# Kernel optimization log

Measured on AMD Instinct MI355X. Metric: run time of the kernel, lower is better.

## Reference

```python
import jax, jax.numpy as jnp
import numpy as np

V, E, H = 32000, 256, 256  # vocab, embed dim, encoder hidden (decoder hidden = 2H)
B, S, T = 64, 32, 32


def gru_cell(x, h, W_ih, W_hh, b_ih, b_hh):
    # PyTorch GRU cell math. x: (B, in), h: (B, Hd)
    gi = x @ W_ih.T + b_ih
    gh = h @ W_hh.T + b_hh
    i_r, i_z, i_n = jnp.split(gi, 3, axis=-1)
    h_r, h_z, h_n = jnp.split(gh, 3, axis=-1)
    r = jax.nn.sigmoid(i_r + h_r)
    z = jax.nn.sigmoid(i_z + h_z)
    n = jnp.tanh(i_n + r * h_n)
    return (1.0 - z) * n + z * h


def setup_inputs() -> dict:
    key = jax.random.key(0)
    ks = jax.random.split(key, 20)
    s = 0.05
    emb_enc = jax.random.normal(ks[0], (V, E), jnp.float32) * s
    emb_enc = emb_enc.at[0].set(0.0)  # padding_idx=0
    emb_dec = jax.random.normal(ks[1], (V, E), jnp.float32) * s
    emb_dec = emb_dec.at[0].set(0.0)
    inp = {
        "src": jax.random.randint(ks[2], (B, S), 0, V),
        "trg": jax.random.randint(ks[3], (B, T), 0, V),
        "emb_enc": emb_enc,
        # encoder bidirectional GRU (single layer)
        "W_ih_f": jax.random.normal(ks[4], (3 * H, E), jnp.float32) * s,
        "W_hh_f": jax.random.normal(ks[5], (3 * H, H), jnp.float32) * s,
        "b_ih_f": jnp.zeros((3 * H,), jnp.float32),
        "b_hh_f": jnp.zeros((3 * H,), jnp.float32),
        "W_ih_b": jax.random.normal(ks[6], (3 * H, E), jnp.float32) * s,
        "W_hh_b": jax.random.normal(ks[7], (3 * H, H), jnp.float32) * s,
        "b_ih_b": jnp.zeros((3 * H,), jnp.float32),
        "b_hh_b": jnp.zeros((3 * H,), jnp.float32),
        "emb_dec": emb_dec,
        # decoder GRU: input E + 2H, hidden 2H
        "W_ih_d": jax.random.normal(ks[8], (3 * 2 * H, E + 2 * H), jnp.float32) * s,
        "W_hh_d": jax.random.normal(ks[9], (3 * 2 * H, 2 * H), jnp.float32) * s,
        "b_ih_d": jnp.zeros((3 * 2 * H,), jnp.float32),
        "b_hh_d": jnp.zeros((3 * 2 * H,), jnp.float32),
        "fc_W": jax.random.normal(ks[10], (V, 2 * H), jnp.float32) * s,
        "fc_b": jnp.zeros((V,), jnp.float32),
    }
    return inp


def _forward(src, trg, emb_enc, W_ih_f, W_hh_f, b_ih_f, b_hh_f,
             W_ih_b, W_hh_b, b_ih_b, b_hh_b, emb_dec,
             W_ih_d, W_hh_d, b_ih_d, b_hh_d, fc_W, fc_b):
    b, s = src.shape
    t = trg.shape[1]
    x = emb_enc[src]                      # (B,S,E)
    xs = jnp.swapaxes(x, 0, 1)            # (S,B,E)
    h0 = jnp.zeros((b, H), x.dtype)

    def fstep(h, xt):
        h = gru_cell(xt, h, W_ih_f, W_hh_f, b_ih_f, b_hh_f)
        return h, None

    def bstep(h, xt):
        h = gru_cell(xt, h, W_ih_b, W_hh_b, b_ih_b, b_hh_b)
        return h, None

    hf, _ = jax.lax.scan(fstep, h0, xs)
    hb, _ = jax.lax.scan(bstep, h0, xs[::-1])
    context = jnp.concatenate([hf, hb], axis=-1)   # (B,2H) = final bidir hidden

    # teacher_forcing_ratio = 1.0 -> decoder input at step t is trg[:, t-1]
    dec_in = jnp.swapaxes(trg[:, :-1], 0, 1)       # (T-1, B)

    def dstep(h, tok):
        xt = jnp.concatenate([emb_dec[tok], context], axis=-1)  # (B, E+2H)
        h = gru_cell(xt, h, W_ih_d, W_hh_d, b_ih_d, b_hh_d)
        logits = h @ fc_W.T + fc_b                              # (B, V)
        return h, logits

    _, logits = jax.lax.scan(dstep, context, dec_in)  # (T-1, B, V)
    logits = jnp.swapaxes(logits, 0, 1)                # (B, T-1, V)
    outputs = jnp.concatenate(
        [jnp.zeros((b, 1, fc_W.shape[0]), logits.dtype), logits], axis=1)
    return outputs


def reference(src, trg, emb_enc, W_ih_f, W_hh_f, b_ih_f, b_hh_f,
              W_ih_b, W_hh_b, b_ih_b, b_hh_b, emb_dec,
              W_ih_d, W_hh_d, b_ih_d, b_hh_d, fc_W, fc_b):
    return _forward(src, trg, emb_enc, W_ih_f, W_hh_f, b_ih_f, b_hh_f,
                    W_ih_b, W_hh_b, b_ih_b, b_hh_b, emb_dec,
                    W_ih_d, W_hh_d, b_ih_d, b_hh_d, fc_W, fc_b)
```

## Files before the change

kernel.cpp:

```cpp
#include <hip/hip_runtime.h>
#include <cmath>

typedef _Float16 f16;
typedef _Float16 f16x4 __attribute__((ext_vector_type(4)));
typedef _Float16 f16x8 __attribute__((ext_vector_type(8)));
typedef float f32x4 __attribute__((ext_vector_type(4)));
typedef unsigned u32x4 __attribute__((ext_vector_type(4)));
typedef unsigned long long u64;

static constexpr u64 SENT = 0xFFFFFFFFFFFFFFFFULL;

union V4 { u32x4 u; f16x8 h; };

typedef __attribute__((address_space(3))) void lds_t;
typedef const __attribute__((address_space(1))) void gbl_t;

static constexpr size_t OFF_WIHF = 0;
static constexpr size_t OFF_WHHF = OFF_WIHF + 768UL*256*2;
static constexpr size_t OFF_WIHB = OFF_WHHF + 768UL*256*2;
static constexpr size_t OFF_WHHB = OFF_WIHB + 768UL*256*2;
static constexpr size_t OFF_WIHD = OFF_WHHB + 768UL*256*2;
static constexpr size_t OFF_WHHD = OFF_WIHD + 1536UL*768*2;
static constexpr size_t OFF_FCW  = OFF_WHHD + 1536UL*512*2;
static constexpr size_t OFF_XENC = OFF_FCW  + 32000UL*512*2;
static constexpr size_t OFF_XDEC = OFF_XENC + 2048UL*256*2;
static constexpr size_t OFF_GIF  = OFF_XDEC + 1984UL*256*2;
static constexpr size_t OFF_GIB  = OFF_GIF  + 2048UL*768*4;
static constexpr size_t OFF_GITOK= OFF_GIB  + 2048UL*768*4;
static constexpr size_t OFF_CTX32= OFF_GITOK+ 1984UL*1536*4;
static constexpr size_t OFF_CTX16= OFF_CTX32+ 64UL*512*4;
static constexpr size_t OFF_HPP  = OFF_CTX16+ 64UL*512*2;
static constexpr size_t OFF_HALL = OFF_HPP  + 2UL*32*64*256*2;

__device__ __forceinline__ float sigmoidf_(float x) {
  return __builtin_amdgcn_rcpf(1.f + __expf(-x));
}
__device__ __forceinline__ float tanhf_(float x) {
  float xc = fminf(fmaxf(x, -10.f), 10.f);
  float e = __expf(2.f * xc);
  return (e - 1.f) * __builtin_amdgcn_rcpf(e + 1.f);
}

__device__ __forceinline__ void wait_vm0() {
  asm volatile("s_waitcnt vmcnt(0)" ::: "memory");
  __builtin_amdgcn_sched_barrier(0);
}
__device__ __forceinline__ void sth4(f16* p, float a, float b, float c, float d) {
  union { u64 u; f16 h[4]; } t;
  t.h[0] = (f16)a; t.h[1] = (f16)b; t.h[2] = (f16)c; t.h[3] = (f16)d;
  __hip_atomic_store((u64*)p, t.u, __ATOMIC_RELAXED, __HIP_MEMORY_SCOPE_AGENT);
}

__global__ void k_init(const int* __restrict__ srct, const int* __restrict__ trgt,
                       const float* __restrict__ embe, const float* __restrict__ embd,
                       const float* __restrict__ wihf, const float* __restrict__ whhf,
                       const float* __restrict__ wihb, const float* __restrict__ whhb,
                       const float* __restrict__ wihd, const float* __restrict__ whhd,
                       const float* __restrict__ fcw,
                       f16* dWihf, f16* dWhhf, f16* dWihb, f16* dWhhb,
                       f16* dWihd, f16* dWhhd, f16* dFcw,
                       f16* __restrict__ Xenc, f16* __restrict__ Xdec,
                       f16* __restrict__ hpp, f16* __restrict__ Hall,
                       float* __restrict__ out) {
  int b = blockIdx.x, tid = threadIdx.x;
  if (b < 1024) {
    long t = (long)b * 256 + tid;
    const long stride = 1024L * 256;
    for (long i = t; i < 4032L * 64; i += stride) {
      int row = (int)(i >> 6), j4 = (int)(i & 63);
      const float* e; f16* d; int tok;
      if (row < 2048) {
        int s = row >> 6, bb = row & 63;
        tok = srct[bb * 32 + s]; e = embe; d = Xenc + (long)row * 256;
      } else {
        int rd = row - 2048; int tt = rd >> 6, bb = rd & 63;
        tok = trgt[bb * 32 + tt]; e = embd; d = Xdec + (long)rd * 256;
      }
      float4 v = ((const float4*)(e + (long)tok * 256))[j4];
      f16x4 o; o.x = (f16)v.x; o.y = (f16)v.y; o.z = (f16)v.z; o.w = (f16)v.w;
      ((f16x4*)d)[j4] = o;
    }
    for (long i = t; i < 64L * 8000; i += stride) {
      long bb = i / 8000, j = i % 8000;
      ((float4*)(out + bb * 1024000L))[j] = make_float4(0.f, 0.f, 0.f, 0.f);
    }
    u64* H8 = (u64*)Hall;
    if (t < 253952) H8[t] = SENT;
    u64* P8 = (u64*)hpp;
    if (t < 4096) { P8[t] = 0ULL; P8[131072 + t] = 0ULL; }
    if (t < 126976) { P8[4096 + t] = SENT; P8[131072 + 4096 + t] = SENT; }
  } else {
    long cb = b - 1024;
    const long stride = 4672L * 256;
    for (long i = cb * 256 + tid; i < 4784128L; i += stride) {
      const float* s; f16* d; long j = i;
      if (j < 49152L)        { s = wihf; d = dWihf; }
      else if (j < 98304L)   { s = whhf; d = dWhhf; j -= 49152L; }
      else if (j < 147456L)  { s = wihb; d = dWihb; j -= 98304L; }
      else if (j < 196608L)  { s = whhb; d = dWhhb; j -= 147456L; }
      else if (j < 491520L)  { s = wihd; d = dWihd; j -= 196608L; }
      else if (j < 688128L)  { s = whhd; d = dWhhd; j -= 491520L; }
      else                   { s = fcw;  d = dFcw;  j -= 688128L; }
      float4 v = ((const float4*)s)[j];
      f16x4 o; o.x = (f16)v.x; o.y = (f16)v.y; o.z = (f16)v.z; o.w = (f16)v.w;
      ((f16x4*)d)[j] = o;
    }
  }
}

__device__ __forceinline__ void gemm_body(int bx, int by,
                                          const f16* __restrict__ A, int lda,
                                          const f16* __restrict__ B, int ldb,
                                          const float* __restrict__ bias,
                                          float* __restrict__ C, int ldc, int Ksteps) {
  int m0 = bx * 64, n0 = by * 64;
  int lane = threadIdx.x & 63, w = threadIdx.x >> 6;
  int ar = m0 + w * 16 + (lane & 15);
  int koff = (lane >> 4) * 8;
  f32x4 acc[4] = {};
  for (int ks = 0; ks < Ksteps; ks++) {
    f16x8 a = *(const f16x8*)(A + (size_t)ar * lda + ks * 32 + koff);
#pragma unroll
    for (int ni = 0; ni < 4; ni++) {
      const f16* bp = B + (size_t)(n0 + ni * 16 + (lane & 15)) * ldb + ks * 32 + koff;
      f16x8 bfr = *(const f16x8*)bp;
      acc[ni] = __builtin_amdgcn_mfma_f32_16x16x32_f16(a, bfr, acc[ni], 0, 0, 0);
    }
  }
  int dm = m0 + w * 16 + ((lane >> 4) << 2);
  int dn0 = n0 + (lane & 15);
#pragma unroll
  for (int ni = 0; ni < 4; ni++) {
    int n = dn0 + ni * 16;
    float bv = bias ? bias[n] : 0.f;
#pragma unroll
    for (int r = 0; r < 4; r++) C[(size_t)(dm + r) * ldc + n] = acc[ni][r] + bv;
  }
}

__global__ __launch_bounds__(256) void k_gi(const f16* __restrict__ Xenc, const f16* __restrict__ Xdec,
                                            const f16* __restrict__ Wf, const f16* __restrict__ Wb,
                                            const f16* __restrict__ Wd,
                                            const float* __restrict__ bf, const float* __restrict__ bb,
                                            float* __restrict__ giF, float* __restrict__ giB,
                                            float* __restrict__ giTok) {
  int b = blockIdx.x;
  if (b < 384)      gemm_body(b & 31, b >> 5, Xenc, 256, Wf, 256, bf, giF, 768, 8);
  else if (b < 768) { b -= 384; gemm_body(b & 31, b >> 5, Xenc, 256, Wb, 256, bb, giB, 768, 8); }
  else              { b -= 768; gemm_body(b % 31, b / 31, Xdec, 256, Wd, 768, nullptr, giTok, 1536, 8); }
}

__global__ __launch_bounds__(256, 1) void k_enc(
    const float* __restrict__ giF, const float* __restrict__ giB,
    const f16* __restrict__ WhhF, const f16* __restrict__ WhhB,
    const float* __restrict__ bhhF, const float* __restrict__ bhhB,
    f16* __restrict__ hpp, float* __restrict__ ctx32, f16* __restrict__ ctx16) {
  __shared__ f16 W[96 * 256];
  int wg = blockIdx.x;
  int dir = wg >> 3, ns = wg & 7;
  int tid = threadIdx.x, lane = tid & 63, wv = tid >> 6;
  int mTile = wv;
  const float* gi = dir ? giB : giF;
  const f16* Whh = dir ? WhhB : WhhF;
  const float* bhh = dir ? bhhB : bhhF;
  f16* hb = hpp + (size_t)dir * (32 * 64 * 256);
  int lo = lane & 15, hi = lane >> 4;
  int m = mTile * 16 + lo;
  int jb0 = ns * 32 + hi * 4;

#pragma unroll
  for (int c = 0; c < 12; c++) {
    int seg = c * 256 + tid;
    int row = seg >> 5, ck = seg & 31;
    int q = row >> 5, ii = row & 31;
    f16x8 v = *(const f16x8*)(Whh + (size_t)(q * 256 + ns * 32 + ii) * 256 + ck * 8);
    int col = (ck * 8) ^ ((row & 7) << 3);
    *(f16x8*)&W[row * 256 + col] = v;
  }
  __syncthreads();

  float4 bh[3][2];
#pragma unroll
  for (int q = 0; q < 3; q++)
#pragma unroll
    for (int i = 0; i < 2; i++)
      bh[q][i] = *(const float4*)(bhh + q * 256 + jb0 + i * 16);

  float4 ho[2] = {};
  float4 gcur[3][2];
  {
    int s0 = dir ? 31 : 0;
    const float* g0 = gi + (size_t)s0 * (64 * 768);
#pragma unroll
    for (int q = 0; q < 3; q++)
#pragma unroll
      for (int i = 0; i < 2; i++)
        gcur[q][i] = *(const float4*)(g0 + (size_t)m * 768 + q * 256 + jb0 + i * 16);
  }

  const int pj = lane >> 3;
  const int prow = mTile * 16 + (lane & 7);

  for (int s = 0; s < 32; s++) {
    {
      const u64* gp = (const u64*)(hb + (size_t)s * 16384) + (size_t)prow * 64 + pj * 8;
      for (;;) {
        u64 v;
        asm volatile("global_load_dwordx2 %0, %1, off sc0 sc1" : "=v"(v) : "v"(gp));
        asm volatile("s_waitcnt vmcnt(0)" ::: "memory");
        if (__all((int)(v != SENT))) break;
        __builtin_amdgcn_s_sleep(1);
      }
      __builtin_amdgcn_sched_barrier(0);
    }
    V4 hv[8];
    const char* hb8 = (const char*)hb + ((size_t)s * 16384 + (size_t)m * 256 + hi * 8) * 2;
    for (;;) {
#pragma unroll
      for (int ks = 0; ks < 8; ks++)
        asm volatile("global_load_dwordx4 %0, %1, off offset:%2 sc0 sc1"
                     : "=&v"(hv[ks].u) : "v"(hb8), "i"(ks * 64));
      wait_vm0();
      unsigned bad = 0;
#pragma unroll
      for (int ks = 0; ks < 8; ks++) {
        bad |= ((hv[ks].u.x & hv[ks].u.y) == 0xFFFFFFFFu);
        bad |= ((hv[ks].u.z & hv[ks].u.w) == 0xFFFFFFFFu);
      }
      if (!__any((int)bad)) break;
      __builtin_amdgcn_s_sleep(1);
    }
    f32x4 acc[3][2] = {};
#pragma unroll
    for (int ks = 0; ks < 8; ks++) {
#pragma unroll
      for (int q = 0; q < 3; q++)
#pragma unroll
        for (int i = 0; i < 2; i++) {
          int row = q * 32 + i * 16 + lo;
          int col = (ks * 32 + hi * 8) ^ ((row & 7) << 3);
          f16x8 w = *(const f16x8*)&W[row * 256 + col];
          acc[q][i] = __builtin_amdgcn_mfma_f32_16x16x32_f16(w, hv[ks].h, acc[q][i], 0, 0, 0);
        }
    }
#pragma unroll
    for (int i = 0; i < 2; i++) {
      float hvv[4];
#pragma unroll
      for (int r2 = 0; r2 < 4; r2++) {
        float rg = sigmoidf_(((const float*)&gcur[0][i])[r2] + acc[0][i][r2] + ((const float*)&bh[0][i])[r2]);
        float zg = sigmoidf_(((const float*)&gcur[1][i])[r2] + acc[1][i][r2] + ((const float*)&bh[1][i])[r2]);
        float ng = tanhf_(((const float*)&gcur[2][i])[r2] + rg * (acc[2][i][r2] + ((const float*)&bh[2][i])[r2]));
        float hprev = ((const float*)&ho[i])[r2];
        hvv[r2] = (1.f - zg) * ng + zg * hprev;
        ((float*)&ho[i])[r2] = hvv[r2];
      }
      if (s < 31) sth4(hb + (size_t)(s + 1) * 16384 + m * 256 + jb0 + i * 16,
                       hvv[0], hvv[1], hvv[2], hvv[3]);
    }
    if (s < 31) {
      int sn = s + 1;
      int sgin = dir ? (31 - sn) : sn;
      const float* gs = gi + (size_t)sgin * (64 * 768);
#pragma unroll
      for (int q = 0; q < 3; q++)
#pragma unroll
        for (int i = 0; i < 2; i++)
          gcur[q][i] = *(const float4*)(gs + (size_t)m * 768 + q * 256 + jb0 + i * 16);
    }
  }
#pragma unroll
  for (int i = 0; i < 2; i++) {
    int c = dir * 256 + jb0 + i * 16;
    *(float4*)(ctx32 + m * 512 + c) = ho[i];
    union { u64 u; f16 h[4]; } t;
#pragma unroll
    for (int r2 = 0; r2 < 4; r2++) t.h[r2] = (f16)((const float*)&ho[i])[r2];
    *(u64*)(ctx16 + m * 512 + c) = t.u;
  }
}

__global__ __launch_bounds__(256, 1) void k_dec(
    const float* __restrict__ giTok, const f16* __restrict__ Wihd, const float* __restrict__ bihd,
    const f16* __restrict__ Whh, const float* __restrict__ bhh,
    const float* __restrict__ ctx32, const f16* __restrict__ ctx16,
    f16* __restrict__ Hall) {
  __shared__ f16 W[48 * 512];
  int cg = blockIdx.x;
  int tid = threadIdx.x, lane = tid & 63, wv = tid >> 6;
  int mTile = wv;
  int lo = lane & 15, hi = lane >> 4;
  int koff = hi * 8;
  int m = mTile * 16 + lo;
  int j0 = cg * 16 + hi * 4;

#pragma unroll
  for (int c = 0; c < 12; c++) {
    int seg = c * 256 + tid;
    int row = seg >> 6, ck = seg & 63;
    int q = row >> 4, ii = row & 15;
    f16x8 v = *(const f16x8*)(Whh + (size_t)(q * 512 + cg * 16 + ii) * 512 + ck * 8);
    int col = (ck * 8) ^ ((row & 7) << 3);
    *(f16x8*)&W[row * 512 + col] = v;
  }

  f32x4 acx[3] = {};
#pragma unroll
  for (int ks = 0; ks < 16; ks++) {
    f16x8 a = *(const f16x8*)(ctx16 + (size_t)m * 512 + ks * 32 + koff);
#pragma unroll
    for (int q = 0; q < 3; q++) {
      f16x8 w = *(const f16x8*)(Wihd + (size_t)(q * 512 + cg * 16 + lo) * 768 + 256 + ks * 32 + koff);
      acx[q] = __builtin_amdgcn_mfma_f32_16x16x32_f16(w, a, acx[q], 0, 0, 0);
    }
  }
  float b0[4], b1[4], bo2[4], bhn[4];
#pragma unroll
  for (int r2 = 0; r2 < 4; r2++) {
    b0[r2]  = acx[0][r2] + bihd[j0 + r2]        + bhh[j0 + r2];
    b1[r2]  = acx[1][r2] + bihd[512 + j0 + r2]  + bhh[512 + j0 + r2];
    bo2[r2] = acx[2][r2] + bihd[1024 + j0 + r2];
    bhn[r2] = bhh[1024 + j0 + r2];
  }
  float4 ho = *(const float4*)(ctx32 + m * 512 + j0);
  float4 gcur[3];
#pragma unroll
  for (int q = 0; q < 3; q++)
    gcur[q] = *(const float4*)(giTok + (size_t)m * 1536 + q * 512 + j0);
  __syncthreads();

  const int pj = lane >> 1;
  const int prow = mTile * 16 + (lane & 1) * 8;

  for (int t = 0; t < 31; t++) {
    V4 hv[16];
    if (t == 0) {
      const char* cb = (const char*)ctx16 + ((size_t)m * 512 + hi * 8) * 2;
#pragma unroll
      for (int ks = 0; ks < 16; ks++)
        hv[ks].u = *(const u32x4*)(cb + ks * 64);
    } else {
      {
        const u64* gp = (const u64*)(Hall + (size_t)(t - 1) * 32768) + (size_t)prow * 128 + pj * 4;
        for (;;) {
          u64 v;
          asm volatile("global_load_dwordx2 %0, %1, off sc0 sc1" : "=v"(v) : "v"(gp));
          asm volatile("s_waitcnt vmcnt(0)" ::: "memory");
          if (__all((int)(v != SENT))) break;
          __builtin_amdgcn_s_sleep(1);
        }
        __builtin_amdgcn_sched_barrier(0);
      }
      const char* hb8 = (const char*)Hall + ((size_t)(t - 1) * 32768 + (size_t)m * 512 + hi * 8) * 2;
      for (;;) {
#pragma unroll
        for (int ks = 0; ks < 16; ks++)
          asm volatile("global_load_dwordx4 %0, %1, off offset:%2 sc0 sc1"
                       : "=&v"(hv[ks].u) : "v"(hb8), "i"(ks * 64));
        wait_vm0();
        unsigned bad = 0;
#pragma unroll
        for (int ks = 0; ks < 16; ks++) {
          bad |= ((hv[ks].u.x & hv[ks].u.y) == 0xFFFFFFFFu);
          bad |= ((hv[ks].u.z & hv[ks].u.w) == 0xFFFFFFFFu);
        }
        if (!__any((int)bad)) break;
        __builtin_amdgcn_s_sleep(1);
      }
    }
    f32x4 acc[3] = {};
#pragma unroll
    for (int ks = 0; ks < 16; ks++) {
#pragma unroll
      for (int q = 0; q < 3; q++) {
        int row = q * 16 + lo;
        int col = (ks * 32 + hi * 8) ^ ((row & 7) << 3);
        f16x8 w = *(const f16x8*)&W[row * 512 + col];
        acc[q] = __builtin_amdgcn_mfma_f32_16x16x32_f16(w, hv[ks].h, acc[q], 0, 0, 0);
      }
    }
    float hvv[4];
#pragma unroll
    for (int r2 = 0; r2 < 4; r2++) {
      float rg = sigmoidf_(((const float*)&gcur[0])[r2] + acc[0][r2] + b0[r2]);
      float zg = sigmoidf_(((const float*)&gcur[1])[r2] + acc[1][r2] + b1[r2]);
      float ng = tanhf_(((const float*)&gcur[2])[r2] + bo2[r2] + rg * (acc[2][r2] + bhn[r2]));
      float hprev = ((const float*)&ho)[r2];
      hvv[r2] = (1.f - zg) * ng + zg * hprev;
      ((float*)&ho)[r2] = hvv[r2];
    }
    sth4(Hall + (size_t)t * 32768 + (size_t)m * 512 + j0, hvv[0], hvv[1], hvv[2], hvv[3]);
    {
      int tn = (t + 1 < 31) ? t + 1 : 30;
      const float* gs = giTok + (size_t)tn * (64 * 1536);
#pragma unroll
      for (int q = 0; q < 3; q++)
        gcur[q] = *(const float4*)(gs + (size_t)m * 1536 + q * 512 + j0);
    }
  }
}

__global__ __launch_bounds__(256, 2) void k_fc(const f16* __restrict__ Hall, const f16* __restrict__ Wfc,
                                               const float* __restrict__ fcb, float* __restrict__ out) {
  __shared__ f16 As[128 * 64];
  __shared__ f16 Bs[128 * 64];
  int bid = blockIdx.x;
  int bx = bid >> 4;
  int by = bid & 15;
  int m0 = by * 128, n0 = bx * 128;
  int tid = threadIdx.x, lane = tid & 63, wv = tid >> 6;
  int wm = wv >> 1, wn = wv & 1;
  int lo = lane & 15, hi = lane >> 4;
  int srow = lane >> 3, scol = (lane & 7) * 8;
  f32x4 acc[4][4] = {};
  for (int kk = 0; kk < 8; kk++) {
    if (kk) __syncthreads();
#pragma unroll
    for (int c4 = 0; c4 < 4; c4++) {
      int c = wv * 4 + c4;
      const f16* sA = Hall + (size_t)(m0 + c * 8 + srow) * 512 + kk * 64 + scol;
      const f16* sB = Wfc  + (size_t)(n0 + c * 8 + srow) * 512 + kk * 64 + scol;
      __builtin_amdgcn_global_load_lds((gbl_t*)sA, (lds_t*)&As[c * 512], 16, 0, 0);
      __builtin_amdgcn_global_load_lds((gbl_t*)sB, (lds_t*)&Bs[c * 512], 16, 0, 0);
    }
    __syncthreads();
#pragma unroll
    for (int ks = 0; ks < 2; ks++) {
      f16x8 af[4], bf[4];
#pragma unroll
      for (int mi = 0; mi < 4; mi++)
        af[mi] = *(const f16x8*)&As[(wm * 64 + mi * 16 + lo) * 64 + ks * 32 + hi * 8];
#pragma unroll
      for (int ni = 0; ni < 4; ni++)
        bf[ni] = *(const f16x8*)&Bs[(wn * 64 + ni * 16 + lo) * 64 + ks * 32 + hi * 8];
#pragma unroll
      for (int mi = 0; mi < 4; mi++) {
#pragma unroll
        for (int ni = 0; ni < 4; ni++)
          acc[mi][ni] = __builtin_amdgcn_mfma_f32_16x16x32_f16(af[mi], bf[ni], acc[mi][ni], 0, 0, 0);
      }
    }
  }
  int dn0 = n0 + wn * 64 + lo;
  float bv[4];
#pragma unroll
  for (int ni = 0; ni < 4; ni++) bv[ni] = fcb[dn0 + ni * 16];
#pragma unroll
  for (int mi = 0; mi < 4; mi++) {
    int mbase = m0 + wm * 64 + mi * 16 + (hi << 2);
#pragma unroll
    for (int rr = 0; rr < 4; rr++) {
      int mm = mbase + rr;
      if (mm < 1984) {
        int t = mm >> 6, bb = mm & 63;
        float* orow = out + (size_t)bb * 1024000 + (size_t)(t + 1) * 32000;
#pragma unroll
        for (int ni = 0; ni < 4; ni++)
          __builtin_nontemporal_store(acc[mi][ni][rr] + bv[ni], orow + dn0 + ni * 16);
      }
    }
  }
}

extern "C" void kernel_launch(void* const* d_in, const int* in_sizes, int n_in,
                              void* d_out, int out_size, void* d_ws, size_t ws_size,
                              hipStream_t stream) {
  const int*   srct = (const int*)d_in[0];
  const int*   trgt = (const int*)d_in[1];
  const float* embe = (const float*)d_in[2];
  const float* wihf = (const float*)d_in[3];
  const float* whhf = (const float*)d_in[4];
  const float* bihf = (const float*)d_in[5];
  const float* bhhf = (const float*)d_in[6];
  const float* wihb = (const float*)d_in[7];
  const float* whhb = (const float*)d_in[8];
  const float* bihb = (const float*)d_in[9];
  const float* bhhb = (const float*)d_in[10];
  const float* embd = (const float*)d_in[11];
  const float* wihd = (const float*)d_in[12];
  const float* whhd = (const float*)d_in[13];
  const float* bihd = (const float*)d_in[14];
  const float* bhhd = (const float*)d_in[15];
  const float* fcw  = (const float*)d_in[16];
  const float* fcb  = (const float*)d_in[17];
  float* out = (float*)d_out;
  char* ws = (char*)d_ws;

  f16* W_ihf = (f16*)(ws + OFF_WIHF);
  f16* W_hhf = (f16*)(ws + OFF_WHHF);
  f16* W_ihb = (f16*)(ws + OFF_WIHB);
  f16* W_hhb = (f16*)(ws + OFF_WHHB);
  f16* W_ihd = (f16*)(ws + OFF_WIHD);
  f16* W_hhd = (f16*)(ws + OFF_WHHD);
  f16* Wfc   = (f16*)(ws + OFF_FCW);
  f16* Xenc  = (f16*)(ws + OFF_XENC);
  f16* Xdec  = (f16*)(ws + OFF_XDEC);
  float* giF   = (float*)(ws + OFF_GIF);
  float* giB   = (float*)(ws + OFF_GIB);
  float* giTok = (float*)(ws + OFF_GITOK);
  float* ctx32 = (float*)(ws + OFF_CTX32);
  f16*   ctx16 = (f16*)(ws + OFF_CTX16);
  f16*   hpp   = (f16*)(ws + OFF_HPP);
  f16*   Hall  = (f16*)(ws + OFF_HALL);

  k_init<<<5696, 256, 0, stream>>>(srct, trgt, embe, embd,
                                   wihf, whhf, wihb, whhb, wihd, whhd, fcw,
                                   W_ihf, W_hhf, W_ihb, W_hhb, W_ihd, W_hhd, Wfc,
                                   Xenc, Xdec, hpp, Hall, out);
  k_gi<<<1512, 256, 0, stream>>>(Xenc, Xdec, W_ihf, W_ihb, W_ihd, bihf, bihb,
                                 giF, giB, giTok);
  k_enc<<<16, 256, 0, stream>>>(giF, giB, W_hhf, W_hhb, bhhf, bhhb, hpp, ctx32, ctx16);
  k_dec<<<32, 256, 0, stream>>>(giTok, W_ihd, bihd, W_hhd, bhhd, ctx32, ctx16, Hall);
  k_fc<<<4000, 256, 0, stream>>>(Hall, Wfc, fcb, out);
}
```

Baseline: 445.5 us.

## Halve decoder recurrence blocks, giving each block 32 hidden columns

The decoder GRU recurrence now runs on 16 workgroups instead of 32. Each workgroup owns 32 hidden columns, so it caches twice the W_hh slice in LDS and issues twice the MFMAs per step. The goal is to reduce the cross-block spin-wait synchronization per timestep, since fewer producers must publish before the next step can start. The cost is more serial compute per block on the critical path and less parallelism.

```diff
diff --git a/kernel.cpp b/kernel.cpp
--- a/kernel.cpp
+++ b/kernel.cpp
@@ -285,52 +285,61 @@
     const f16* __restrict__ Whh, const float* __restrict__ bhh,
     const float* __restrict__ ctx32, const f16* __restrict__ ctx16,
     f16* __restrict__ Hall) {
-  __shared__ f16 W[48 * 512];
-  int cg = blockIdx.x;
+  __shared__ f16 W[96 * 512];
+  int cg2 = blockIdx.x;
   int tid = threadIdx.x, lane = tid & 63, wv = tid >> 6;
   int mTile = wv;
   int lo = lane & 15, hi = lane >> 4;
   int koff = hi * 8;
   int m = mTile * 16 + lo;
-  int j0 = cg * 16 + hi * 4;
-
-#pragma unroll
-  for (int c = 0; c < 12; c++) {
+  int jb0 = cg2 * 32 + hi * 4;
+
+#pragma unroll
+  for (int c = 0; c < 24; c++) {
     int seg = c * 256 + tid;
     int row = seg >> 6, ck = seg & 63;
-    int q = row >> 4, ii = row & 15;
-    f16x8 v = *(const f16x8*)(Whh + (size_t)(q * 512 + cg * 16 + ii) * 512 + ck * 8);
+    int q = row >> 5, ii = row & 31;
+    f16x8 v = *(const f16x8*)(Whh + (size_t)(q * 512 + cg2 * 32 + ii) * 512 + ck * 8);
     int col = (ck * 8) ^ ((row & 7) << 3);
     *(f16x8*)&W[row * 512 + col] = v;
   }
 
-  f32x4 acx[3] = {};
+  f32x4 acx[3][2] = {};
 #pragma unroll
   for (int ks = 0; ks < 16; ks++) {
     f16x8 a = *(const f16x8*)(ctx16 + (size_t)m * 512 + ks * 32 + koff);
 #pragma unroll
-    for (int q = 0; q < 3; q++) {
-      f16x8 w = *(const f16x8*)(Wihd + (size_t)(q * 512 + cg * 16 + lo) * 768 + 256 + ks * 32 + koff);
-      acx[q] = __builtin_amdgcn_mfma_f32_16x16x32_f16(w, a, acx[q], 0, 0, 0);
-    }
-  }
-  float b0[4], b1[4], bo2[4], bhn[4];
-#pragma unroll
-  for (int r2 = 0; r2 < 4; r2++) {
-    b0[r2]  = acx[0][r2] + bihd[j0 + r2]        + bhh[j0 + r2];
-    b1[r2]  = acx[1][r2] + bihd[512 + j0 + r2]  + bhh[512 + j0 + r2];
-    bo2[r2] = acx[2][r2] + bihd[1024 + j0 + r2];
-    bhn[r2] = bhh[1024 + j0 + r2];
-  }
-  float4 ho = *(const float4*)(ctx32 + m * 512 + j0);
-  float4 gcur[3];
+    for (int q = 0; q < 3; q++)
+#pragma unroll
+      for (int i = 0; i < 2; i++) {
+        f16x8 w = *(const f16x8*)(Wihd + (size_t)(q * 512 + cg2 * 32 + i * 16 + lo) * 768 + 256 + ks * 32 + koff);
+        acx[q][i] = __builtin_amdgcn_mfma_f32_16x16x32_f16(w, a, acx[q][i], 0, 0, 0);
+      }
+  }
+  float b0[2][4], b1[2][4], bo2[2][4], bhn[2][4];
+#pragma unroll
+  for (int i = 0; i < 2; i++)
+#pragma unroll
+    for (int r2 = 0; r2 < 4; r2++) {
+      int j = jb0 + i * 16 + r2;
+      b0[i][r2]  = acx[0][i][r2] + bihd[j]        + bhh[j];
+      b1[i][r2]  = acx[1][i][r2] + bihd[512 + j]  + bhh[512 + j];
+      bo2[i][r2] = acx[2][i][r2] + bihd[1024 + j];
+      bhn[i][r2] = bhh[1024 + j];
+    }
+  float4 ho[2];
+  float4 gcur[3][2];
+#pragma unroll
+  for (int i = 0; i < 2; i++) ho[i] = *(const float4*)(ctx32 + m * 512 + jb0 + i * 16);
 #pragma unroll
   for (int q = 0; q < 3; q++)
-    gcur[q] = *(const float4*)(giTok + (size_t)m * 1536 + q * 512 + j0);
+#pragma unroll
+    for (int i = 0; i < 2; i++)
+      gcur[q][i] = *(const float4*)(giTok + (size_t)m * 1536 + q * 512 + jb0 + i * 16);
   __syncthreads();
 
-  const int pj = lane >> 1;
-  const int prow = mTile * 16 + (lane & 1) * 8;
+  const int pp = lane >> 2;
+  const int prow = mTile * 16 + (lane & 3) * 4;
 
   for (int t = 0; t < 31; t++) {
     V4 hv[16];
@@ -341,7 +350,7 @@
         hv[ks].u = *(const u32x4*)(cb + ks * 64);
     } else {
       {
-        const u64* gp = (const u64*)(Hall + (size_t)(t - 1) * 32768) + (size_t)prow * 128 + pj * 4;
+        const u64* gp = (const u64*)(Hall + (size_t)(t - 1) * 32768) + (size_t)prow * 128 + pp * 8;
         for (;;) {
           u64 v;
           asm volatile("global_load_dwordx2 %0, %1, off sc0 sc1" : "=v"(v) : "v"(gp));
@@ -368,34 +377,42 @@
         __builtin_amdgcn_s_sleep(1);
       }
     }
-    f32x4 acc[3] = {};
+    f32x4 acc[3][2] = {};
 #pragma unroll
     for (int ks = 0; ks < 16; ks++) {
 #pragma unroll
-      for (int q = 0; q < 3; q++) {
-        int row = q * 16 + lo;
-        int col = (ks * 32 + hi * 8) ^ ((row & 7) << 3);
-        f16x8 w = *(const f16x8*)&W[row * 512 + col];
-        acc[q] = __builtin_amdgcn_mfma_f32_16x16x32_f16(w, hv[ks].h, acc[q], 0, 0, 0);
-      }
-    }
-    float hvv[4];
-#pragma unroll
-    for (int r2 = 0; r2 < 4; r2++) {
-      float rg = sigmoidf_(((const float*)&gcur[0])[r2] + acc[0][r2] + b0[r2]);
-      float zg = sigmoidf_(((const float*)&gcur[1])[r2] + acc[1][r2] + b1[r2]);
-      float ng = tanhf_(((const float*)&gcur[2])[r2] + bo2[r2] + rg * (acc[2][r2] + bhn[r2]));
-      float hprev = ((const float*)&ho)[r2];
-      hvv[r2] = (1.f - zg) * ng + zg * hprev;
-      ((float*)&ho)[r2] = hvv[r2];
-    }
-    sth4(Hall + (size_t)t * 32768 + (size_t)m * 512 + j0, hvv[0], hvv[1], hvv[2], hvv[3]);
+      for (int q = 0; q < 3; q++)
+#pragma unroll
+        for (int i = 0; i < 2; i++) {
+          int row = q * 32 + i * 16 + lo;
+          int col = (ks * 32 + hi * 8) ^ ((row & 7) << 3);
+          f16x8 w = *(const f16x8*)&W[row * 512 + col];
+          acc[q][i] = __builtin_amdgcn_mfma_f32_16x16x32_f16(w, hv[ks].h, acc[q][i], 0, 0, 0);
+        }
+    }
+#pragma unroll
+    for (int i = 0; i < 2; i++) {
+      float hvv[4];
+#pragma unroll
+      for (int r2 = 0; r2 < 4; r2++) {
+        float rg = sigmoidf_(((const float*)&gcur[0][i])[r2] + acc[0][i][r2] + b0[i][r2]);
+        float zg = sigmoidf_(((const float*)&gcur[1][i])[r2] + acc[1][i][r2] + b1[i][r2]);
+        float ng = tanhf_(((const float*)&gcur[2][i])[r2] + bo2[i][r2] + rg * (acc[2][i][r2] + bhn[i][r2]));
+        float hprev = ((const float*)&ho[i])[r2];
+        hvv[r2] = (1.f - zg) * ng + zg * hprev;
+        ((float*)&ho[i])[r2] = hvv[r2];
+      }
+      sth4(Hall + (size_t)t * 32768 + (size_t)m * 512 + jb0 + i * 16,
+           hvv[0], hvv[1], hvv[2], hvv[3]);
+    }
     {
       int tn = (t + 1 < 31) ? t + 1 : 30;
       const float* gs = giTok + (size_t)tn * (64 * 1536);
 #pragma unroll
       for (int q = 0; q < 3; q++)
-        gcur[q] = *(const float4*)(gs + (size_t)m * 1536 + q * 512 + j0);
+#pragma unroll
+        for (int i = 0; i < 2; i++)
+          gcur[q][i] = *(const float4*)(gs + (size_t)m * 1536 + q * 512 + jb0 + i * 16);
     }
   }
 }
@@ -510,6 +527,6 @@
   k_gi<<<1512, 256, 0, stream>>>(Xenc, Xdec, W_ihf, W_ihb, W_ihd, bihf, bihb,
                                  giF, giB, giTok);
   k_enc<<<16, 256, 0, stream>>>(giF, giB, W_hhf, W_hhb, bhhf, bhhb, hpp, ctx32, ctx16);
-  k_dec<<<32, 256, 0, stream>>>(giTok, W_ihd, bihd, W_hhd, bhhd, ctx32, ctx16, Hall);
+  k_dec<<<16, 256, 0, stream>>>(giTok, W_ihd, bihd, W_hhd, bhhd, ctx32, ctx16, Hall);
   k_fc<<<4000, 256, 0, stream>>>(Hall, Wfc, fcb, out);
 }
```

Result: slower. 493.7 us (+10.8%).

## Fuse encoder and decoder recurrences into one kernel with sentinel-based context handoff

Applied to the files above, without the earlier changes.

Merges the encoder and decoder GRU kernels into a single 48-block launch. Decoder blocks preload their weights into LDS, then spin on sentinel-initialized fp16 context entries that the encoder writes with atomic stores. This removes a kernel boundary and overlaps decoder setup with the encoder recurrence. It also drops the per-step sentinel poll in the encoder loop and the fp32 context buffer, so the decoder's initial hidden state is now read from fp16, which loses some precision. Correctness depends on all 48 blocks being co-resident so the spin-wait cannot deadlock.

```diff
diff --git a/kernel.cpp b/kernel.cpp
--- a/kernel.cpp
+++ b/kernel.cpp
@@ -27,8 +27,7 @@
 static constexpr size_t OFF_GIF  = OFF_XDEC + 1984UL*256*2;
 static constexpr size_t OFF_GIB  = OFF_GIF  + 2048UL*768*4;
 static constexpr size_t OFF_GITOK= OFF_GIB  + 2048UL*768*4;
-static constexpr size_t OFF_CTX32= OFF_GITOK+ 1984UL*1536*4;
-static constexpr size_t OFF_CTX16= OFF_CTX32+ 64UL*512*4;
+static constexpr size_t OFF_CTX16= OFF_GITOK+ 1984UL*1536*4;
 static constexpr size_t OFF_HPP  = OFF_CTX16+ 64UL*512*2;
 static constexpr size_t OFF_HALL = OFF_HPP  + 2UL*32*64*256*2;
 
@@ -61,7 +60,7 @@
                        f16* dWihd, f16* dWhhd, f16* dFcw,
                        f16* __restrict__ Xenc, f16* __restrict__ Xdec,
                        f16* __restrict__ hpp, f16* __restrict__ Hall,
-                       float* __restrict__ out) {
+                       f16* __restrict__ ctx16, float* __restrict__ out) {
   int b = blockIdx.x, tid = threadIdx.x;
   if (b < 1024) {
     long t = (long)b * 256 + tid;
@@ -89,6 +88,8 @@
     u64* P8 = (u64*)hpp;
     if (t < 4096) { P8[t] = 0ULL; P8[131072 + t] = 0ULL; }
     if (t < 126976) { P8[4096 + t] = SENT; P8[131072 + 4096 + t] = SENT; }
+    u64* C8 = (u64*)ctx16;
+    if (t < 8192) C8[t] = SENT;
   } else {
     long cb = b - 1024;
     const long stride = 4672L * 256;
@@ -150,12 +151,12 @@
   else              { b -= 768; gemm_body(b % 31, b / 31, Xdec, 256, Wd, 768, nullptr, giTok, 1536, 8); }
 }
 
-__global__ __launch_bounds__(256, 1) void k_enc(
+__device__ __forceinline__ void enc_body(
+    f16* W,
     const float* __restrict__ giF, const float* __restrict__ giB,
     const f16* __restrict__ WhhF, const f16* __restrict__ WhhB,
     const float* __restrict__ bhhF, const float* __restrict__ bhhB,
-    f16* __restrict__ hpp, float* __restrict__ ctx32, f16* __restrict__ ctx16) {
-  __shared__ f16 W[96 * 256];
+    f16* __restrict__ hpp, f16* __restrict__ ctx16) {
   int wg = blockIdx.x;
   int dir = wg >> 3, ns = wg & 7;
   int tid = threadIdx.x, lane = tid & 63, wv = tid >> 6;
@@ -198,21 +199,7 @@
         gcur[q][i] = *(const float4*)(g0 + (size_t)m * 768 + q * 256 + jb0 + i * 16);
   }
 
-  const int pj = lane >> 3;
-  const int prow = mTile * 16 + (lane & 7);
-
   for (int s = 0; s < 32; s++) {
-    {
-      const u64* gp = (const u64*)(hb + (size_t)s * 16384) + (size_t)prow * 64 + pj * 8;
-      for (;;) {
-        u64 v;
-        asm volatile("global_load_dwordx2 %0, %1, off sc0 sc1" : "=v"(v) : "v"(gp));
-        asm volatile("s_waitcnt vmcnt(0)" ::: "memory");
-        if (__all((int)(v != SENT))) break;
-        __builtin_amdgcn_s_sleep(1);
-      }
-      __builtin_amdgcn_sched_barrier(0);
-    }
     V4 hv[8];
     const char* hb8 = (const char*)hb + ((size_t)s * 16384 + (size_t)m * 256 + hi * 8) * 2;
     for (;;) {
@@ -272,21 +259,17 @@
 #pragma unroll
   for (int i = 0; i < 2; i++) {
     int c = dir * 256 + jb0 + i * 16;
-    *(float4*)(ctx32 + m * 512 + c) = ho[i];
-    union { u64 u; f16 h[4]; } t;
-#pragma unroll
-    for (int r2 = 0; r2 < 4; r2++) t.h[r2] = (f16)((const float*)&ho[i])[r2];
-    *(u64*)(ctx16 + m * 512 + c) = t.u;
-  }
-}
-
-__global__ __launch_bounds__(256, 1) void k_dec(
+    sth4(ctx16 + m * 512 + c, ((const float*)&ho[i])[0], ((const float*)&ho[i])[1],
+         ((const float*)&ho[i])[2], ((const float*)&ho[i])[3]);
+  }
+}
+
+__device__ __forceinline__ void dec_body(
+    f16* W,
     const float* __restrict__ giTok, const f16* __restrict__ Wihd, const float* __restrict__ bihd,
     const f16* __restrict__ Whh, const float* __restrict__ bhh,
-    const float* __restrict__ ctx32, const f16* __restrict__ ctx16,
-    f16* __restrict__ Hall) {
-  __shared__ f16 W[48 * 512];
-  int cg = blockIdx.x;
+    const f16* __restrict__ ctx16, f16* __restrict__ Hall) {
+  int cg = blockIdx.x - 16;
   int tid = threadIdx.x, lane = tid & 63, wv = tid >> 6;
   int mTile = wv;
   int lo = lane & 15, hi = lane >> 4;
@@ -303,43 +286,69 @@
     int col = (ck * 8) ^ ((row & 7) << 3);
     *(f16x8*)&W[row * 512 + col] = v;
   }
-
-  f32x4 acx[3] = {};
-#pragma unroll
-  for (int ks = 0; ks < 16; ks++) {
-    f16x8 a = *(const f16x8*)(ctx16 + (size_t)m * 512 + ks * 32 + koff);
-#pragma unroll
-    for (int q = 0; q < 3; q++) {
-      f16x8 w = *(const f16x8*)(Wihd + (size_t)(q * 512 + cg * 16 + lo) * 768 + 256 + ks * 32 + koff);
-      acx[q] = __builtin_amdgcn_mfma_f32_16x16x32_f16(w, a, acx[q], 0, 0, 0);
-    }
-  }
-  float b0[4], b1[4], bo2[4], bhn[4];
+  float bi0[4], bi1[4], bi2[4], bh0[4], bh1[4], bhn[4];
 #pragma unroll
   for (int r2 = 0; r2 < 4; r2++) {
-    b0[r2]  = acx[0][r2] + bihd[j0 + r2]        + bhh[j0 + r2];
-    b1[r2]  = acx[1][r2] + bihd[512 + j0 + r2]  + bhh[512 + j0 + r2];
-    bo2[r2] = acx[2][r2] + bihd[1024 + j0 + r2];
-    bhn[r2] = bhh[1024 + j0 + r2];
-  }
-  float4 ho = *(const float4*)(ctx32 + m * 512 + j0);
+    bi0[r2] = bihd[j0 + r2];        bh0[r2] = bhh[j0 + r2];
+    bi1[r2] = bihd[512 + j0 + r2];  bh1[r2] = bhh[512 + j0 + r2];
+    bi2[r2] = bihd[1024 + j0 + r2]; bhn[r2] = bhh[1024 + j0 + r2];
+  }
   float4 gcur[3];
 #pragma unroll
   for (int q = 0; q < 3; q++)
     gcur[q] = *(const float4*)(giTok + (size_t)m * 1536 + q * 512 + j0);
   __syncthreads();
 
+  V4 hv[16];
+  {
+    const char* cb8 = (const char*)ctx16 + ((size_t)m * 512 + hi * 8) * 2;
+    for (;;) {
+#pragma unroll
+      for (int ks = 0; ks < 16; ks++)
+        asm volatile("global_load_dwordx4 %0, %1, off offset:%2 sc0 sc1"
+                     : "=&v"(hv[ks].u) : "v"(cb8), "i"(ks * 64));
+      wait_vm0();
+      unsigned bad = 0;
+#pragma unroll
+      for (int ks = 0; ks < 16; ks++) {
+        bad |= ((hv[ks].u.x & hv[ks].u.y) == 0xFFFFFFFFu);
+        bad |= ((hv[ks].u.z & hv[ks].u.w) == 0xFFFFFFFFu);
+      }
+      if (!__any((int)bad)) break;
+      __builtin_amdgcn_s_sleep(32);
+    }
+  }
+  float4 ho;
+  {
+    u64 hoq;
+    const u64* hp = (const u64*)(ctx16 + (size_t)m * 512 + j0);
+    asm volatile("global_load_dwordx2 %0, %1, off sc0 sc1" : "=v"(hoq) : "v"(hp));
+    asm volatile("s_waitcnt vmcnt(0)" ::: "memory");
+    union { u64 u; f16 h[4]; } hu; hu.u = hoq;
+    ho = make_float4((float)hu.h[0], (float)hu.h[1], (float)hu.h[2], (float)hu.h[3]);
+  }
+  f32x4 acx[3] = {};
+#pragma unroll
+  for (int ks = 0; ks < 16; ks++) {
+#pragma unroll
+    for (int q = 0; q < 3; q++) {
+      f16x8 w = *(const f16x8*)(Wihd + (size_t)(q * 512 + cg * 16 + lo) * 768 + 256 + ks * 32 + koff);
+      acx[q] = __builtin_amdgcn_mfma_f32_16x16x32_f16(w, hv[ks].h, acx[q], 0, 0, 0);
+    }
+  }
+  float b0[4], b1[4], bo2[4];
+#pragma unroll
+  for (int r2 = 0; r2 < 4; r2++) {
+    b0[r2]  = acx[0][r2] + bi0[r2] + bh0[r2];
+    b1[r2]  = acx[1][r2] + bi1[r2] + bh1[r2];
+    bo2[r2] = acx[2][r2] + bi2[r2];
+  }
+
   const int pj = lane >> 1;
   const int prow = mTile * 16 + (lane & 1) * 8;
 
   for (int t = 0; t < 31; t++) {
-    V4 hv[16];
-    if (t == 0) {
-      const char* cb = (const char*)ctx16 + ((size_t)m * 512 + hi * 8) * 2;
-#pragma unroll
-      for (int ks = 0; ks < 16; ks++)
-        hv[ks].u = *(const u32x4*)(cb + ks * 64);
-    } else {
+    if (t > 0) {
       {
         const u64* gp = (const u64*)(Hall + (size_t)(t - 1) * 32768) + (size_t)prow * 128 + pj * 4;
         for (;;) {
@@ -398,6 +407,21 @@
         gcur[q] = *(const float4*)(gs + (size_t)m * 1536 + q * 512 + j0);
     }
   }
+}
+
+__global__ __launch_bounds__(256, 1) void k_encdec(
+    const float* __restrict__ giF, const float* __restrict__ giB,
+    const f16* __restrict__ WhhF, const f16* __restrict__ WhhB,
+    const float* __restrict__ bhhF, const float* __restrict__ bhhB,
+    f16* __restrict__ hpp, f16* __restrict__ ctx16,
+    const float* __restrict__ giTok, const f16* __restrict__ Wihd, const float* __restrict__ bihd,
+    const f16* __restrict__ Whhd, const float* __restrict__ bhhd,
+    f16* __restrict__ Hall) {
+  __shared__ f16 W[96 * 256];
+  if (blockIdx.x < 16)
+    enc_body(W, giF, giB, WhhF, WhhB, bhhF, bhhB, hpp, ctx16);
+  else
+    dec_body(W, giTok, Wihd, bihd, Whhd, bhhd, ctx16, Hall);
 }
 
 __global__ __launch_bounds__(256, 2) void k_fc(const f16* __restrict__ Hall, const f16* __restrict__ Wfc,
@@ -498,7 +522,6 @@
   float* giF   = (float*)(ws + OFF_GIF);
   float* giB   = (float*)(ws + OFF_GIB);
   float* giTok = (float*)(ws + OFF_GITOK);
-  float* ctx32 = (float*)(ws + OFF_CTX32);
   f16*   ctx16 = (f16*)(ws + OFF_CTX16);
   f16*   hpp   = (f16*)(ws + OFF_HPP);
   f16*   Hall  = (f16*)(ws + OFF_HALL);
@@ -506,10 +529,10 @@
   k_init<<<5696, 256, 0, stream>>>(srct, trgt, embe, embd,
                                    wihf, whhf, wihb, whhb, wihd, whhd, fcw,
                                    W_ihf, W_hhf, W_ihb, W_hhb, W_ihd, W_hhd, Wfc,
-                                   Xenc, Xdec, hpp, Hall, out);
+                                   Xenc, Xdec, hpp, Hall, ctx16, out);
   k_gi<<<1512, 256, 0, stream>>>(Xenc, Xdec, W_ihf, W_ihb, W_ihd, bihf, bihb,
                                  giF, giB, giTok);
-  k_enc<<<16, 256, 0, stream>>>(giF, giB, W_hhf, W_hhb, bhhf, bhhb, hpp, ctx32, ctx16);
-  k_dec<<<32, 256, 0, stream>>>(giTok, W_ihd, bihd, W_hhd, bhhd, ctx32, ctx16, Hall);
+  k_encdec<<<48, 256, 0, stream>>>(giF, giB, W_hhf, W_hhb, bhhf, bhhb, hpp, ctx16,
+                                   giTok, W_ihd, bihd, W_hhd, bhhd, Hall);
   k_fc<<<4000, 256, 0, stream>>>(Hall, Wfc, fcb, out);
 }
```

After: 415.5 us. 1.07x faster.
